# Kernel optimization log

Hardware: AMD Instinct MI355X
Metric: run time of the kernel (lower is better)

## Reference

```python
import jax, jax.numpy as jnp
import numpy as np

V, D, L, H, F, S = 32000, 1024, 6, 16, 4096, 1024
B, T = 2, 1024
DH = D // H
EPS = 1e-5


def layer_norm(x, w, b):
    m = jnp.mean(x, axis=-1, keepdims=True)
    v = jnp.var(x, axis=-1, keepdims=True)
    return (x - m) * jax.lax.rsqrt(v + EPS) * w + b


def setup_inputs() -> dict:
    key = jax.random.key(0)
    ks = jax.random.split(key, 12)
    n = lambda k, shape: jax.random.normal(k, shape, jnp.float32) * 0.02
    return {
        "idx": jax.random.randint(ks[0], (B, T), 0, V),
        "tok_emb": n(ks[1], (V, D)),
        "pos_emb": n(ks[2], (S, D)),
        "ln1_w": jnp.ones((L, D), jnp.float32),
        "ln1_b": jnp.zeros((L, D), jnp.float32),
        "wq": n(ks[3], (L, D, D)),
        "wk": n(ks[4], (L, D, D)),
        "wv": n(ks[5], (L, D, D)),
        "proj": n(ks[6], (L, D, D)),
        "ln2_w": jnp.ones((L, D), jnp.float32),
        "ln2_b": jnp.zeros((L, D), jnp.float32),
        "fc1_w": n(ks[7], (L, F, D)),
        "fc1_b": jnp.zeros((L, F), jnp.float32),
        "fc2_w": n(ks[8], (L, D, F)),
        "fc2_b": jnp.zeros((L, D), jnp.float32),
        "lnf_w": jnp.ones((D,), jnp.float32),
        "lnf_b": jnp.zeros((D,), jnp.float32),
        "head_w": n(ks[9], (V, D)),
    }


def reference(idx, tok_emb, pos_emb, ln1_w, ln1_b, wq, wk, wv, proj,
              ln2_w, ln2_b, fc1_w, fc1_b, fc2_w, fc2_b, lnf_w, lnf_b, head_w):
    b, t = idx.shape
    x = tok_emb[idx] + pos_emb[:t][None, :, :]  # [B,T,D]
    causal = jnp.tril(jnp.ones((t, t), bool))

    def block(x, p):
        l1w, l1b, Wq, Wk, Wv, Wp, l2w, l2b, F1w, F1b, F2w, F2b = p
        h = layer_norm(x, l1w, l1b)
        q = (h @ Wq.T).reshape(b, t, H, DH).transpose(0, 2, 1, 3)  # [B,H,T,dh]
        k = (h @ Wk.T).reshape(b, t, H, DH).transpose(0, 2, 1, 3)
        v = (h @ Wv.T).reshape(b, t, H, DH).transpose(0, 2, 1, 3)
        # muP attention: 1/d_head scaling (not 1/sqrt(d_head))
        att = jnp.einsum('bhqd,bhkd->bhqk', q, k) * (1.0 / DH)
        att = jnp.where(causal, att, -jnp.inf)
        att = jax.nn.softmax(att, axis=-1)
        y = jnp.einsum('bhqk,bhkd->bhqd', att, v)
        y = y.transpose(0, 2, 1, 3).reshape(b, t, D)
        x = x + y @ Wp.T
        h = layer_norm(x, l2w, l2b)
        h = jax.nn.gelu(h @ F1w.T + F1b, approximate=False)  # torch F.gelu = exact erf
        x = x + (h @ F2w.T + F2b)
        return x, None

    x, _ = jax.lax.scan(block, x, (ln1_w, ln1_b, wq, wk, wv, proj,
                                   ln2_w, ln2_b, fc1_w, fc1_b, fc2_w, fc2_b))
    x = layer_norm(x, lnf_w, lnf_b)
    return x @ head_w.T  # [B,T,V] logits (MuReadout with unit multipliers)
```

## Files before the change

kernel.cpp:

```cpp
#include <hip/hip_runtime.h>
#include <cmath>

typedef __bf16 bf16_t;
typedef bf16_t bf16x8 __attribute__((ext_vector_type(8)));
typedef bf16_t bf16x4 __attribute__((ext_vector_type(4)));
typedef float floatx4 __attribute__((ext_vector_type(4)));

#define B_ 2
#define T_ 1024
#define D_ 1024
#define H_ 16
#define DH_ 64
#define L_ 6
#define F_ 4096
#define V_ 32000
#define NTOK (B_ * T_)

__global__ __launch_bounds__(256) void detect_kernel(
    const unsigned short* __restrict__ tok, int* __restrict__ flag)
{
  __shared__ int cnt;
  if (threadIdx.x == 0) cnt = 0;
  __syncthreads();
  int c = 0;
#pragma unroll
  for (int i = 0; i < 16; i++) {
    unsigned short h = tok[threadIdx.x * 16 + i];
    int e = (h >> 7) & 0xFF;
    if (e >= 134) c++;
  }
  atomicAdd(&cnt, c);
  __syncthreads();
  if (threadIdx.x == 0) *flag = (cnt > 64) ? 1 : 0;
}

__device__ inline bf16x8 load8(const void* p, size_t i, int fp32m) {
  bf16x8 r;
  if (fp32m) {
    const float* f = (const float*)p + i;
    float4 v0 = *(const float4*)f;
    float4 v1 = *(const float4*)(f + 4);
    r[0] = (bf16_t)v0.x; r[1] = (bf16_t)v0.y; r[2] = (bf16_t)v0.z; r[3] = (bf16_t)v0.w;
    r[4] = (bf16_t)v1.x; r[5] = (bf16_t)v1.y; r[6] = (bf16_t)v1.z; r[7] = (bf16_t)v1.w;
  } else {
    r = *(const bf16x8*)((const bf16_t*)p + i);
  }
  return r;
}

__device__ inline float loadf(const void* p, size_t i, int fp32m) {
  return fp32m ? ((const float*)p)[i] : (float)((const bf16_t*)p)[i];
}

__global__ __launch_bounds__(256) void convflat_kernel(
    const void* __restrict__ src, bf16_t* __restrict__ dst,
    const int* __restrict__ modep, long n)
{
  int fp32m = *modep;
  size_t i = ((size_t)blockIdx.x * 256 + threadIdx.x) * 8;
  if ((long)i >= n) return;
  bf16x8 r = load8(src, i, fp32m);
  *(bf16x8*)(dst + i) = r;
}

__global__ __launch_bounds__(256) void convqkv_kernel(
    const void* __restrict__ wq, const void* __restrict__ wk,
    const void* __restrict__ wv, bf16_t* __restrict__ dst,
    const int* __restrict__ modep)
{
  int fp32m = *modep;
  size_t i = ((size_t)blockIdx.x * 256 + threadIdx.x) * 8;
  const size_t per = (size_t)D_ * D_;
  int lm = (int)(i / per);
  size_t off = i - (size_t)lm * per;
  int l = lm / 3, mat = lm - l * 3;
  const void* src = (mat == 0) ? wq : ((mat == 1) ? wk : wv);
  bf16x8 r = load8(src, (size_t)l * per + off, fp32m);
  *(bf16x8*)(dst + i) = r;
}

__global__ __launch_bounds__(256) void embed_kernel(
    const int* __restrict__ idx, const void* __restrict__ tok,
    const void* __restrict__ pos, float* __restrict__ x,
    const int* __restrict__ modep)
{
  int fp32m = *modep;
  int row = blockIdx.x;
  int t = row & (T_ - 1);
  int tokid = idx[row];
  int c = threadIdx.x * 4;
  float tv[4], pv[4];
  if (fp32m) {
    float4 a = *(const float4*)((const float*)tok + (size_t)tokid * D_ + c);
    float4 b = *(const float4*)((const float*)pos + (size_t)t * D_ + c);
    tv[0] = a.x; tv[1] = a.y; tv[2] = a.z; tv[3] = a.w;
    pv[0] = b.x; pv[1] = b.y; pv[2] = b.z; pv[3] = b.w;
  } else {
    bf16x4 a = *(const bf16x4*)((const bf16_t*)tok + (size_t)tokid * D_ + c);
    bf16x4 b = *(const bf16x4*)((const bf16_t*)pos + (size_t)t * D_ + c);
#pragma unroll
    for (int j = 0; j < 4; j++) { tv[j] = (float)a[j]; pv[j] = (float)b[j]; }
  }
  float4 o;
  o.x = tv[0] + pv[0]; o.y = tv[1] + pv[1];
  o.z = tv[2] + pv[2]; o.w = tv[3] + pv[3];
  *(float4*)(x + (size_t)row * D_ + c) = o;
}

__global__ __launch_bounds__(256) void ln_kernel(
    const float* __restrict__ x, const void* __restrict__ w,
    const void* __restrict__ bb, bf16_t* __restrict__ out,
    const int* __restrict__ modep, int woff)
{
  int fp32m = *modep;
  int row = blockIdx.x, tid = threadIdx.x;
  int lane = tid & 63, wid = tid >> 6;
  const float* xr = x + (size_t)row * D_;
  float4 xv = ((const float4*)xr)[tid];
  float s = xv.x + xv.y + xv.z + xv.w;
  float sq = xv.x * xv.x + xv.y * xv.y + xv.z * xv.z + xv.w * xv.w;
#pragma unroll
  for (int off = 32; off; off >>= 1) {
    s += __shfl_xor(s, off);
    sq += __shfl_xor(sq, off);
  }
  __shared__ float ss[4], ssq[4];
  if (lane == 0) { ss[wid] = s; ssq[wid] = sq; }
  __syncthreads();
  s = ss[0] + ss[1] + ss[2] + ss[3];
  sq = ssq[0] + ssq[1] + ssq[2] + ssq[3];
  float mean = s * (1.f / D_);
  float var = sq * (1.f / D_) - mean * mean;
  var = fmaxf(var, 0.f);
  float rstd = rsqrtf(var + 1e-5f);
  int c = tid * 4;
  float xa[4] = {xv.x, xv.y, xv.z, xv.w};
  bf16x4 ov;
#pragma unroll
  for (int j = 0; j < 4; j++) {
    float wj = loadf(w, (size_t)woff + c + j, fp32m);
    float bj = loadf(bb, (size_t)woff + c + j, fp32m);
    ov[j] = (bf16_t)((xa[j] - mean) * rstd * wj + bj);
  }
  *(bf16x4*)(out + (size_t)row * D_ + c) = ov;
}

__device__ inline float gelu_f(float v) {
  return 0.5f * v * (1.f + erff(v * 0.70710678118654752f));
}

__device__ inline void gload16(void* lds, const void* g) {
  __builtin_amdgcn_global_load_lds(
      (__attribute__((address_space(1))) void*)(g),
      (__attribute__((address_space(3))) void*)(lds), 16, 0, 0);
}

__global__ __launch_bounds__(256) void gemm128(
    const bf16_t* __restrict__ A, const bf16_t* __restrict__ W,
    const void* __restrict__ bias, size_t boff, const float* __restrict__ res,
    bf16_t* __restrict__ outb, float* __restrict__ outf, void* __restrict__ outx,
    const int* __restrict__ modep, int M, int N, int K, int dogelu)
{
  __shared__ __align__(16) bf16_t As[128 * 32];
  __shared__ __align__(16) bf16_t Bs[128 * 32];
  int fp32m = *modep;
  int tid = threadIdx.x;
  int lane = tid & 63, wid = tid >> 6;
  int wm = wid & 1, wn = wid >> 1;
  int m0 = blockIdx.x * 128, n0 = blockIdx.y * 128;
  int ln15 = lane & 15, q4 = lane >> 4;
  int srow = tid >> 2;
  int scol = (tid & 3) * 8;
  const bf16_t* Ag0 = A + (size_t)(m0 + srow) * K + scol;
  const bf16_t* Ag1 = A + (size_t)(m0 + 64 + srow) * K + scol;
  const bf16_t* Wg0 = W + (size_t)(n0 + srow) * K + scol;
  const bf16_t* Wg1 = W + (size_t)(n0 + 64 + srow) * K + scol;
  bf16_t* Asp0 = &As[tid * 8];
  bf16_t* Asp1 = &As[2048 + tid * 8];
  bf16_t* Bsp0 = &Bs[tid * 8];
  bf16_t* Bsp1 = &Bs[2048 + tid * 8];
  floatx4 acc[4][4] = {};
  for (int k0 = 0; k0 < K; k0 += 32) {
    __syncthreads();
    gload16(Asp0, Ag0 + k0);
    gload16(Asp1, Ag1 + k0);
    gload16(Bsp0, Wg0 + k0);
    gload16(Bsp1, Wg1 + k0);
    __syncthreads();
    bf16x8 a[4], b[4];
#pragma unroll
    for (int i = 0; i < 4; i++) {
      a[i] = *(const bf16x8*)&As[(wm * 64 + i * 16 + ln15) * 32 + q4 * 8];
      b[i] = *(const bf16x8*)&Bs[(wn * 64 + i * 16 + ln15) * 32 + q4 * 8];
    }
#pragma unroll
    for (int mt = 0; mt < 4; mt++)
#pragma unroll
      for (int nt = 0; nt < 4; nt++)
        acc[mt][nt] = __builtin_amdgcn_mfma_f32_16x16x32_bf16(a[mt], b[nt], acc[mt][nt], 0, 0, 0);
  }
#pragma unroll
  for (int mt = 0; mt < 4; mt++)
#pragma unroll
    for (int nt = 0; nt < 4; nt++) {
      int col = n0 + wn * 64 + nt * 16 + ln15;
      float bv = bias ? loadf(bias, boff + col, fp32m) : 0.f;
#pragma unroll
      for (int r = 0; r < 4; r++) {
        int row = m0 + wm * 64 + mt * 16 + q4 * 4 + r;
        float v = acc[mt][nt][r] + bv;
        if (dogelu) v = gelu_f(v);
        size_t o = (size_t)row * N + col;
        if (res) v += res[o];
        if (outf) outf[o] = v;
        if (outb) outb[o] = (bf16_t)v;
        if (outx) {
          if (fp32m) ((float*)outx)[o] = v;
          else ((bf16_t*)outx)[o] = (bf16_t)v;
        }
      }
    }
}

__global__ __launch_bounds__(256) void gemm_bt(
    const bf16_t* __restrict__ A, const void* __restrict__ W, size_t woffs,
    const void* __restrict__ bias, size_t boff, const float* __restrict__ res,
    bf16_t* __restrict__ outb, float* __restrict__ outf, void* __restrict__ outx,
    const int* __restrict__ modep, int M, int N, int K, int dogelu)
{
  __shared__ __align__(16) bf16_t As[64][40];
  __shared__ __align__(16) bf16_t Bs[64][40];
  int fp32m = *modep;
  int tid = threadIdx.x;
  int lane = tid & 63, wid = tid >> 6;
  int wm = wid & 1, wn = wid >> 1;
  int m0 = blockIdx.y * 64, n0 = blockIdx.x * 64;
  int srow = tid >> 2, scol = (tid & 3) * 8;
  const bf16_t* Ap = A + (size_t)(m0 + srow) * K + scol;
  size_t wrow = woffs + (size_t)(n0 + srow) * K + scol;
  floatx4 acc[2][2] = {};
  int ln15 = lane & 15, q4 = lane >> 4;
  for (int k0 = 0; k0 < K; k0 += 32) {
    __syncthreads();
    *(bf16x8*)&As[srow][scol] = *(const bf16x8*)(Ap + k0);
    *(bf16x8*)&Bs[srow][scol] = load8(W, wrow + k0, fp32m);
    __syncthreads();
    bf16x8 a0 = *(const bf16x8*)&As[wm * 32 + ln15][q4 * 8];
    bf16x8 a1 = *(const bf16x8*)&As[wm * 32 + 16 + ln15][q4 * 8];
    bf16x8 b0 = *(const bf16x8*)&Bs[wn * 32 + ln15][q4 * 8];
    bf16x8 b1 = *(const bf16x8*)&Bs[wn * 32 + 16 + ln15][q4 * 8];
    acc[0][0] = __builtin_amdgcn_mfma_f32_16x16x32_bf16(a0, b0, acc[0][0], 0, 0, 0);
    acc[0][1] = __builtin_amdgcn_mfma_f32_16x16x32_bf16(a0, b1, acc[0][1], 0, 0, 0);
    acc[1][0] = __builtin_amdgcn_mfma_f32_16x16x32_bf16(a1, b0, acc[1][0], 0, 0, 0);
    acc[1][1] = __builtin_amdgcn_mfma_f32_16x16x32_bf16(a1, b1, acc[1][1], 0, 0, 0);
  }
#pragma unroll
  for (int mt = 0; mt < 2; mt++)
#pragma unroll
    for (int nt = 0; nt < 2; nt++) {
      int col = n0 + wn * 32 + nt * 16 + ln15;
      float bv = bias ? loadf(bias, boff + col, fp32m) : 0.f;
#pragma unroll
      for (int r = 0; r < 4; r++) {
        int row = m0 + wm * 32 + mt * 16 + q4 * 4 + r;
        float v = acc[mt][nt][r] + bv;
        if (dogelu) v = gelu_f(v);
        size_t o = (size_t)row * N + col;
        if (res) v += res[o];
        if (outf) outf[o] = v;
        if (outb) outb[o] = (bf16_t)v;
        if (outx) {
          if (fp32m) ((float*)outx)[o] = v;
          else ((bf16_t*)outx)[o] = (bf16_t)v;
        }
      }
    }
}

__global__ __launch_bounds__(256) void attn_mfma(
    const bf16_t* __restrict__ qkv, bf16_t* __restrict__ y)
{
  __shared__ __align__(16) bf16_t Ks[64][72];
  __shared__ __align__(16) bf16_t Vt[64][72];
  __shared__ __align__(16) bf16_t Ps[4][16][72];
  int tid = threadIdx.x;
  int lane = tid & 63, w = tid >> 6;
  int ln15 = lane & 15, g = lane >> 4;
  int idxb = blockIdx.x;
  int phase = idxb >> 8, slot = idxb & 255;
  int bh = slot >> 3, jj = slot & 7;
  int qb = phase ? jj : (15 - jj);
  int b = bh >> 4, h = bh & 15;
  int q0 = qb * 64;
  int qrow = q0 + w * 16;
  const bf16_t* kp = qkv + 1024;
  const bf16_t* vp = qkv + 2048;
  bf16x8 qa0, qa1;
  {
    size_t base = ((size_t)(b * T_ + qrow + ln15)) * 3072 + h * 64 + g * 8;
    qa0 = *(const bf16x8*)(qkv + base);
    qa1 = *(const bf16x8*)(qkv + base + 32);
  }
  floatx4 o[4] = {};
  float m_i[4], l_i[4];
#pragma unroll
  for (int r = 0; r < 4; r++) { m_i[r] = -__builtin_inff(); l_i[r] = 0.f; }
  int ntile = qb + 1;
  int sr = tid >> 2, sc = (tid & 3) * 16;
  for (int it = 0; it < ntile; it++) {
    int k0 = it * 64;
    __syncthreads();
    size_t gb = ((size_t)(b * T_ + k0 + sr)) * 3072 + h * 64 + sc;
    bf16x8 kv0 = *(const bf16x8*)(kp + gb);
    bf16x8 kv1 = *(const bf16x8*)(kp + gb + 8);
    bf16x8 vv0 = *(const bf16x8*)(vp + gb);
    bf16x8 vv1 = *(const bf16x8*)(vp + gb + 8);
    *(bf16x8*)&Ks[sr][sc] = kv0;
    *(bf16x8*)&Ks[sr][sc + 8] = kv1;
#pragma unroll
    for (int e = 0; e < 8; e++) {
      int d0 = sc + e, d1 = sc + 8 + e;
      Vt[d0][sr ^ (((d0 >> 3) & 7) << 3)] = vv0[e];
      Vt[d1][sr ^ (((d1 >> 3) & 7) << 3)] = vv1[e];
    }
    __syncthreads();
    floatx4 s[4] = {};
#pragma unroll
    for (int nt = 0; nt < 4; nt++) {
      bf16x8 b0 = *(const bf16x8*)&Ks[nt * 16 + ln15][g * 8];
      bf16x8 b1 = *(const bf16x8*)&Ks[nt * 16 + ln15][32 + g * 8];
      s[nt] = __builtin_amdgcn_mfma_f32_16x16x32_bf16(qa0, b0, s[nt], 0, 0, 0);
      s[nt] = __builtin_amdgcn_mfma_f32_16x16x32_bf16(qa1, b1, s[nt], 0, 0, 0);
    }
    int last = (it == ntile - 1);
    float p[4][4];
    float mt[4];
#pragma unroll
    for (int r = 0; r < 4; r++) mt[r] = -__builtin_inff();
#pragma unroll
    for (int nt = 0; nt < 4; nt++)
#pragma unroll
      for (int r = 0; r < 4; r++) {
        float sv = s[nt][r] * 0.015625f;
        if (last && (k0 + nt * 16 + ln15) > (qrow + g * 4 + r))
          sv = -__builtin_inff();
        p[nt][r] = sv;
        mt[r] = fmaxf(mt[r], sv);
      }
#pragma unroll
    for (int off = 1; off < 16; off <<= 1)
#pragma unroll
      for (int r = 0; r < 4; r++) mt[r] = fmaxf(mt[r], __shfl_xor(mt[r], off));
    float alpha[4];
#pragma unroll
    for (int r = 0; r < 4; r++) {
      float mn = fmaxf(m_i[r], mt[r]);
      alpha[r] = __expf(m_i[r] - mn);
      m_i[r] = mn;
    }
    float rs[4] = {0.f, 0.f, 0.f, 0.f};
#pragma unroll
    for (int nt = 0; nt < 4; nt++)
#pragma unroll
      for (int r = 0; r < 4; r++) {
        float pv = __expf(p[nt][r] - m_i[r]);
        rs[r] += pv;
        Ps[w][g * 4 + r][nt * 16 + ln15] = (bf16_t)pv;
      }
#pragma unroll
    for (int off = 1; off < 16; off <<= 1)
#pragma unroll
      for (int r = 0; r < 4; r++) rs[r] += __shfl_xor(rs[r], off);
#pragma unroll
    for (int r = 0; r < 4; r++) l_i[r] = l_i[r] * alpha[r] + rs[r];
#pragma unroll
    for (int nt = 0; nt < 4; nt++)
#pragma unroll
      for (int r = 0; r < 4; r++) o[nt][r] *= alpha[r];
#pragma unroll
    for (int ks = 0; ks < 2; ks++) {
      bf16x8 pa = *(const bf16x8*)&Ps[w][ln15][ks * 32 + g * 8];
#pragma unroll
      for (int nt = 0; nt < 4; nt++) {
        int d = nt * 16 + ln15;
        bf16x8 vb = *(const bf16x8*)&Vt[d][(ks * 32 + g * 8) ^ (((d >> 3) & 7) << 3)];
        o[nt] = __builtin_amdgcn_mfma_f32_16x16x32_bf16(pa, vb, o[nt], 0, 0, 0);
      }
    }
  }
#pragma unroll
  for (int nt = 0; nt < 4; nt++)
#pragma unroll
    for (int r = 0; r < 4; r++) {
      size_t orow = (size_t)(b * T_ + qrow + g * 4 + r) * D_ + h * 64 + nt * 16 + ln15;
      y[orow] = (bf16_t)(o[nt][r] / l_i[r]);
    }
}

__global__ __launch_bounds__(256) void attn_kernel(
    const bf16_t* __restrict__ q, const bf16_t* __restrict__ k,
    const bf16_t* __restrict__ v, bf16_t* __restrict__ y, int stride)
{
  __shared__ float Kt[64][65];
  __shared__ float Vt[64][65];
  __shared__ float qs[4][64];
  __shared__ float ps[4][64];
  int tid = threadIdx.x;
  int lane = tid & 63, w = tid >> 6;
  int blk = blockIdx.x;
  int tqblk = blk & 255;
  int bh = blk >> 8;
  int b = bh >> 4, hh = bh & 15;
  int tq_base = tqblk * 4;
  int tq = tq_base + w;
  size_t qrow = ((size_t)(b * T_ + tq)) * stride + hh * DH_;
  qs[w][lane] = (float)q[qrow + lane];
  float m_i = -INFINITY, l_i = 0.f, acc = 0.f;
  int ntiles = (tq_base >> 6) + 1;
  int lr = tid >> 2, lc = (tid & 3) * 16;
  for (int it = 0; it < ntiles; it++) {
    int tk0 = it * 64;
    __syncthreads();
    size_t gbase = ((size_t)(b * T_ + tk0 + lr)) * stride + hh * DH_ + lc;
    bf16x8 kv0 = *(const bf16x8*)(k + gbase);
    bf16x8 kv1 = *(const bf16x8*)(k + gbase + 8);
    bf16x8 vv0 = *(const bf16x8*)(v + gbase);
    bf16x8 vv1 = *(const bf16x8*)(v + gbase + 8);
#pragma unroll
    for (int j = 0; j < 8; j++) {
      Kt[lr][lc + j] = (float)kv0[j];
      Kt[lr][lc + 8 + j] = (float)kv1[j];
      Vt[lr][lc + j] = (float)vv0[j];
      Vt[lr][lc + 8 + j] = (float)vv1[j];
    }
    __syncthreads();
    int tk = tk0 + lane;
    float s = -INFINITY;
    if (tk <= tq) {
      float a = 0.f;
#pragma unroll
      for (int d = 0; d < 64; d++) a += qs[w][d] * Kt[lane][d];
      s = a * (1.f / 64.f);
    }
    float mt = s;
#pragma unroll
    for (int off = 32; off; off >>= 1) mt = fmaxf(mt, __shfl_xor(mt, off));
    float mnew = fmaxf(m_i, mt);
    float alpha = (m_i == -INFINITY) ? 0.f : expf(m_i - mnew);
    float p = (tk <= tq) ? expf(s - mnew) : 0.f;
    float psum = p;
#pragma unroll
    for (int off = 32; off; off >>= 1) psum += __shfl_xor(psum, off);
    l_i = l_i * alpha + psum;
    ps[w][lane] = p;
    float pv = 0.f;
#pragma unroll
    for (int j = 0; j < 64; j++) pv += ps[w][j] * Vt[j][lane];
    acc = acc * alpha + pv;
    m_i = mnew;
  }
  y[((size_t)(b * T_ + tq)) * D_ + hh * DH_ + lane] = (bf16_t)(acc / l_i);
}

static inline void launch_gemm128(const bf16_t* A, const bf16_t* W,
                                  const void* bias, size_t boff, const float* res,
                                  bf16_t* outb, float* outf, void* outx,
                                  const int* modep, int M, int N, int K,
                                  int dogelu, hipStream_t s)
{
  dim3 g(M / 128, N / 128);
  gemm128<<<g, dim3(256), 0, s>>>(A, W, bias, boff, res, outb, outf, outx,
                                  modep, M, N, K, dogelu);
}

static inline void launch_gemm_old(const bf16_t* A, const void* W, size_t woffs,
                                   const void* bias, size_t boff, const float* res,
                                   bf16_t* outb, float* outf, void* outx,
                                   const int* modep, int M, int N, int K,
                                   int dogelu, hipStream_t s)
{
  dim3 g(N / 64, M / 64);
  gemm_bt<<<g, dim3(256), 0, s>>>(A, W, woffs, bias, boff, res, outb, outf,
                                  outx, modep, M, N, K, dogelu);
}

#define OFF_X      256ull
#define OFF_H      8388864ull
#define OFF_QKV    12583168ull
#define OFF_Y      25166080ull
#define OFF_HF     29360384ull
#define OFF_WQKV   46137600ull
#define OFF_WPROJ  83886336ull
#define OFF_WFC1   96469248ull
#define OFF_WFC2   146800896ull
#define OFF_WHEAD  197132544ull
#define REQ_WS     262668544ull

extern "C" void kernel_launch(void* const* d_in, const int* in_sizes, int n_in,
                              void* d_out, int out_size, void* d_ws, size_t ws_size,
                              hipStream_t stream)
{
  (void)in_sizes; (void)n_in; (void)out_size;
  const int* idx      = (const int*)d_in[0];
  const void* tok_emb = d_in[1];
  const void* pos_emb = d_in[2];
  const void* ln1_w   = d_in[3];
  const void* ln1_b   = d_in[4];
  const void* wq      = d_in[5];
  const void* wk      = d_in[6];
  const void* wv      = d_in[7];
  const void* wproj   = d_in[8];
  const void* ln2_w   = d_in[9];
  const void* ln2_b   = d_in[10];
  const void* fc1_w   = d_in[11];
  const void* fc1_b   = d_in[12];
  const void* fc2_w   = d_in[13];
  const void* fc2_b   = d_in[14];
  const void* lnf_w   = d_in[15];
  const void* lnf_b   = d_in[16];
  const void* head_w  = d_in[17];

  char* ws = (char*)d_ws;
  int* modep = (int*)ws;
  detect_kernel<<<1, 256, 0, stream>>>((const unsigned short*)tok_emb, modep);

  if (ws_size >= REQ_WS) {
    float*  x   = (float*)(ws + OFF_X);
    bf16_t* h   = (bf16_t*)(ws + OFF_H);
    bf16_t* qkv = (bf16_t*)(ws + OFF_QKV);
    bf16_t* yb  = (bf16_t*)(ws + OFF_Y);
    bf16_t* hf  = (bf16_t*)(ws + OFF_HF);
    bf16_t* wqkvb = (bf16_t*)(ws + OFF_WQKV);
    bf16_t* wprjb = (bf16_t*)(ws + OFF_WPROJ);
    bf16_t* wfc1b = (bf16_t*)(ws + OFF_WFC1);
    bf16_t* wfc2b = (bf16_t*)(ws + OFF_WFC2);
    bf16_t* whedb = (bf16_t*)(ws + OFF_WHEAD);

    convqkv_kernel<<<9216, 256, 0, stream>>>(wq, wk, wv, wqkvb, modep);
    convflat_kernel<<<3072, 256, 0, stream>>>(wproj, wprjb, modep, (long)L_ * D_ * D_);
    convflat_kernel<<<12288, 256, 0, stream>>>(fc1_w, wfc1b, modep, (long)L_ * F_ * D_);
    convflat_kernel<<<12288, 256, 0, stream>>>(fc2_w, wfc2b, modep, (long)L_ * D_ * F_);
    convflat_kernel<<<16000, 256, 0, stream>>>(head_w, whedb, modep, (long)V_ * D_);

    embed_kernel<<<NTOK, 256, 0, stream>>>(idx, tok_emb, pos_emb, x, modep);

    for (int l = 0; l < L_; l++) {
      size_t wd = (size_t)l * D_ * D_;
      size_t wf = (size_t)l * F_ * D_;
      ln_kernel<<<NTOK, 256, 0, stream>>>(x, ln1_w, ln1_b, h, modep, l * D_);
      launch_gemm128(h, wqkvb + (size_t)l * 3 * D_ * D_, nullptr, 0, nullptr,
                     qkv, nullptr, nullptr, modep, NTOK, 3 * D_, D_, 0, stream);
      attn_mfma<<<512, 256, 0, stream>>>(qkv, yb);
      launch_gemm128(yb, wprjb + wd, nullptr, 0, x, nullptr, x, nullptr,
                     modep, NTOK, D_, D_, 0, stream);
      ln_kernel<<<NTOK, 256, 0, stream>>>(x, ln2_w, ln2_b, h, modep, l * D_);
      launch_gemm128(h, wfc1b + wf, fc1_b, (size_t)l * F_, nullptr, hf, nullptr,
                     nullptr, modep, NTOK, F_, D_, 1, stream);
      launch_gemm128(hf, wfc2b + wf, fc2_b, (size_t)l * D_, x, nullptr, x,
                     nullptr, modep, NTOK, D_, F_, 0, stream);
    }

    ln_kernel<<<NTOK, 256, 0, stream>>>(x, lnf_w, lnf_b, h, modep, 0);
    launch_gemm128(h, whedb, nullptr, 0, nullptr, nullptr, nullptr, d_out,
                   modep, NTOK, V_, D_, 0, stream);
  } else {
    float*  x  = (float*)(ws + 256);
    bf16_t* h  = (bf16_t*)(ws + 8388864);
    bf16_t* qb = (bf16_t*)(ws + 12583168);
    bf16_t* kb = (bf16_t*)(ws + 16777472);
    bf16_t* vb = (bf16_t*)(ws + 20971776);
    bf16_t* yb = (bf16_t*)(ws + 25166080);
    bf16_t* hf = (bf16_t*)(ws + 29360384);

    embed_kernel<<<NTOK, 256, 0, stream>>>(idx, tok_emb, pos_emb, x, modep);

    for (int l = 0; l < L_; l++) {
      size_t wd = (size_t)l * D_ * D_;
      size_t wf = (size_t)l * F_ * D_;
      ln_kernel<<<NTOK, 256, 0, stream>>>(x, ln1_w, ln1_b, h, modep, l * D_);
      launch_gemm_old(h, wq, wd, nullptr, 0, nullptr, qb, nullptr, nullptr,
                      modep, NTOK, D_, D_, 0, stream);
      launch_gemm_old(h, wk, wd, nullptr, 0, nullptr, kb, nullptr, nullptr,
                      modep, NTOK, D_, D_, 0, stream);
      launch_gemm_old(h, wv, wd, nullptr, 0, nullptr, vb, nullptr, nullptr,
                      modep, NTOK, D_, D_, 0, stream);
      attn_kernel<<<B_ * H_ * (T_ / 4), 256, 0, stream>>>(qb, kb, vb, yb, D_);
      launch_gemm_old(yb, wproj, wd, nullptr, 0, x, nullptr, x, nullptr,
                      modep, NTOK, D_, D_, 0, stream);
      ln_kernel<<<NTOK, 256, 0, stream>>>(x, ln2_w, ln2_b, h, modep, l * D_);
      launch_gemm_old(h, fc1_w, wf, fc1_b, (size_t)l * F_, nullptr, hf, nullptr,
                      nullptr, modep, NTOK, F_, D_, 1, stream);
      launch_gemm_old(hf, fc2_w, wf, fc2_b, (size_t)l * D_, x, nullptr, x,
                      nullptr, modep, NTOK, D_, F_, 0, stream);
    }

    ln_kernel<<<NTOK, 256, 0, stream>>>(x, lnf_w, lnf_b, h, modep, 0);
    launch_gemm_old(h, head_w, 0, nullptr, 0, nullptr, nullptr, nullptr, d_out,
                    modep, NTOK, V_, D_, 0, stream);
  }
}
```

Measured before the change: 2.644 ms.

## Template GEMM tile sizes and remap workgroups across XCDs for L2 locality

Turns the fixed 128x128 GEMM into a BM x BN template and gives each projection its own tile shape: smaller tiles for the narrow-N projection and fc2 GEMMs, so they launch more workgroups on the many CUs. It also switches to a 1D grid whose block ids are remapped so consecutive workgroups on the same XCD cover neighbouring M tiles of one N column, aiming for better L2 reuse of weight tiles. Smaller tiles cost more reloads of operands per FLOP and lower MFMA density per wave.

```diff
diff --git a/kernel.cpp b/kernel.cpp
--- a/kernel.cpp
+++ b/kernel.cpp
@@ -155,59 +155,68 @@
       (__attribute__((address_space(3))) void*)(lds), 16, 0, 0);
 }
 
-__global__ __launch_bounds__(256) void gemm128(
+template<int BM, int BN>
+__global__ __launch_bounds__(256) void gemm_t(
     const bf16_t* __restrict__ A, const bf16_t* __restrict__ W,
     const void* __restrict__ bias, size_t boff, const float* __restrict__ res,
     bf16_t* __restrict__ outb, float* __restrict__ outf, void* __restrict__ outx,
-    const int* __restrict__ modep, int M, int N, int K, int dogelu)
-{
-  __shared__ __align__(16) bf16_t As[128 * 32];
-  __shared__ __align__(16) bf16_t Bs[128 * 32];
+    const int* __restrict__ modep, int M, int N, int K, int dogelu, int mshift)
+{
+  constexpr int MT = BM / 32, NT = BN / 32;
+  __shared__ __align__(16) bf16_t As[BM * 32];
+  __shared__ __align__(16) bf16_t Bs[BN * 32];
   int fp32m = *modep;
   int tid = threadIdx.x;
   int lane = tid & 63, wid = tid >> 6;
   int wm = wid & 1, wn = wid >> 1;
-  int m0 = blockIdx.x * 128, n0 = blockIdx.y * 128;
+  int nwg = gridDim.x, bid = blockIdx.x;
+  int qq = nwg >> 3, rr = nwg & 7;
+  int xcd = bid & 7, ii = bid >> 3;
+  int wg = (xcd < rr ? xcd * (qq + 1) : rr * (qq + 1) + (xcd - rr) * qq) + ii;
+  int m0 = (wg & ((1 << mshift) - 1)) * BM;
+  int n0 = (wg >> mshift) * BN;
   int ln15 = lane & 15, q4 = lane >> 4;
-  int srow = tid >> 2;
-  int scol = (tid & 3) * 8;
-  const bf16_t* Ag0 = A + (size_t)(m0 + srow) * K + scol;
-  const bf16_t* Ag1 = A + (size_t)(m0 + 64 + srow) * K + scol;
-  const bf16_t* Wg0 = W + (size_t)(n0 + srow) * K + scol;
-  const bf16_t* Wg1 = W + (size_t)(n0 + 64 + srow) * K + scol;
-  bf16_t* Asp0 = &As[tid * 8];
-  bf16_t* Asp1 = &As[2048 + tid * 8];
-  bf16_t* Bsp0 = &Bs[tid * 8];
-  bf16_t* Bsp1 = &Bs[2048 + tid * 8];
-  floatx4 acc[4][4] = {};
+  int srow = tid >> 2, scol = (tid & 3) * 8;
+  const bf16_t* Ag[BM / 64];
+  const bf16_t* Wg[BN / 64];
+#pragma unroll
+  for (int hh = 0; hh < BM / 64; hh++)
+    Ag[hh] = A + (size_t)(m0 + hh * 64 + srow) * K + scol;
+#pragma unroll
+  for (int hh = 0; hh < BN / 64; hh++)
+    Wg[hh] = W + (size_t)(n0 + hh * 64 + srow) * K + scol;
+  floatx4 acc[MT][NT] = {};
   for (int k0 = 0; k0 < K; k0 += 32) {
     __syncthreads();
-    gload16(Asp0, Ag0 + k0);
-    gload16(Asp1, Ag1 + k0);
-    gload16(Bsp0, Wg0 + k0);
-    gload16(Bsp1, Wg1 + k0);
-    __syncthreads();
-    bf16x8 a[4], b[4];
-#pragma unroll
-    for (int i = 0; i < 4; i++) {
-      a[i] = *(const bf16x8*)&As[(wm * 64 + i * 16 + ln15) * 32 + q4 * 8];
-      b[i] = *(const bf16x8*)&Bs[(wn * 64 + i * 16 + ln15) * 32 + q4 * 8];
-    }
-#pragma unroll
-    for (int mt = 0; mt < 4; mt++)
-#pragma unroll
-      for (int nt = 0; nt < 4; nt++)
+#pragma unroll
+    for (int hh = 0; hh < BM / 64; hh++)
+      gload16(&As[hh * 2048 + tid * 8], Ag[hh] + k0);
+#pragma unroll
+    for (int hh = 0; hh < BN / 64; hh++)
+      gload16(&Bs[hh * 2048 + tid * 8], Wg[hh] + k0);
+    __syncthreads();
+    bf16x8 a[MT], b[NT];
+#pragma unroll
+    for (int i = 0; i < MT; i++)
+      a[i] = *(const bf16x8*)&As[(wm * (BM / 2) + i * 16 + ln15) * 32 + q4 * 8];
+#pragma unroll
+    for (int j = 0; j < NT; j++)
+      b[j] = *(const bf16x8*)&Bs[(wn * (BN / 2) + j * 16 + ln15) * 32 + q4 * 8];
+#pragma unroll
+    for (int mt = 0; mt < MT; mt++)
+#pragma unroll
+      for (int nt = 0; nt < NT; nt++)
         acc[mt][nt] = __builtin_amdgcn_mfma_f32_16x16x32_bf16(a[mt], b[nt], acc[mt][nt], 0, 0, 0);
   }
 #pragma unroll
-  for (int mt = 0; mt < 4; mt++)
-#pragma unroll
-    for (int nt = 0; nt < 4; nt++) {
-      int col = n0 + wn * 64 + nt * 16 + ln15;
+  for (int mt = 0; mt < MT; mt++)
+#pragma unroll
+    for (int nt = 0; nt < NT; nt++) {
+      int col = n0 + wn * (BN / 2) + nt * 16 + ln15;
       float bv = bias ? loadf(bias, boff + col, fp32m) : 0.f;
 #pragma unroll
       for (int r = 0; r < 4; r++) {
-        int row = m0 + wm * 64 + mt * 16 + q4 * 4 + r;
+        int row = m0 + wm * (BM / 2) + mt * 16 + q4 * 4 + r;
         float v = acc[mt][nt][r] + bv;
         if (dogelu) v = gelu_f(v);
         size_t o = (size_t)row * N + col;
@@ -462,15 +471,18 @@
   y[((size_t)(b * T_ + tq)) * D_ + hh * DH_ + lane] = (bf16_t)(acc / l_i);
 }
 
-static inline void launch_gemm128(const bf16_t* A, const bf16_t* W,
-                                  const void* bias, size_t boff, const float* res,
-                                  bf16_t* outb, float* outf, void* outx,
-                                  const int* modep, int M, int N, int K,
-                                  int dogelu, hipStream_t s)
-{
-  dim3 g(M / 128, N / 128);
-  gemm128<<<g, dim3(256), 0, s>>>(A, W, bias, boff, res, outb, outf, outx,
-                                  modep, M, N, K, dogelu);
+template<int BM, int BN>
+static inline void launch_gemm_t(const bf16_t* A, const bf16_t* W,
+                                 const void* bias, size_t boff, const float* res,
+                                 bf16_t* outb, float* outf, void* outx,
+                                 const int* modep, int M, int N, int K,
+                                 int dogelu, hipStream_t s)
+{
+  int nMB = M / BM;
+  int mshift = (nMB == 16) ? 4 : ((nMB == 32) ? 5 : 31 - __builtin_clz(nMB));
+  int nwg = nMB * (N / BN);
+  gemm_t<BM, BN><<<dim3(nwg), dim3(256), 0, s>>>(
+      A, W, bias, boff, res, outb, outf, outx, modep, M, N, K, dogelu, mshift);
 }
 
 static inline void launch_gemm_old(const bf16_t* A, const void* W, size_t woffs,
@@ -548,21 +560,22 @@
       size_t wd = (size_t)l * D_ * D_;
       size_t wf = (size_t)l * F_ * D_;
       ln_kernel<<<NTOK, 256, 0, stream>>>(x, ln1_w, ln1_b, h, modep, l * D_);
-      launch_gemm128(h, wqkvb + (size_t)l * 3 * D_ * D_, nullptr, 0, nullptr,
-                     qkv, nullptr, nullptr, modep, NTOK, 3 * D_, D_, 0, stream);
+      launch_gemm_t<64, 128>(h, wqkvb + (size_t)l * 3 * D_ * D_, nullptr, 0,
+                             nullptr, qkv, nullptr, nullptr, modep,
+                             NTOK, 3 * D_, D_, 0, stream);
       attn_mfma<<<512, 256, 0, stream>>>(qkv, yb);
-      launch_gemm128(yb, wprjb + wd, nullptr, 0, x, nullptr, x, nullptr,
-                     modep, NTOK, D_, D_, 0, stream);
+      launch_gemm_t<64, 64>(yb, wprjb + wd, nullptr, 0, x, nullptr, x, nullptr,
+                            modep, NTOK, D_, D_, 0, stream);
       ln_kernel<<<NTOK, 256, 0, stream>>>(x, ln2_w, ln2_b, h, modep, l * D_);
-      launch_gemm128(h, wfc1b + wf, fc1_b, (size_t)l * F_, nullptr, hf, nullptr,
-                     nullptr, modep, NTOK, F_, D_, 1, stream);
-      launch_gemm128(hf, wfc2b + wf, fc2_b, (size_t)l * D_, x, nullptr, x,
-                     nullptr, modep, NTOK, D_, F_, 0, stream);
+      launch_gemm_t<128, 128>(h, wfc1b + wf, fc1_b, (size_t)l * F_, nullptr, hf,
+                              nullptr, nullptr, modep, NTOK, F_, D_, 1, stream);
+      launch_gemm_t<64, 64>(hf, wfc2b + wf, fc2_b, (size_t)l * D_, x, nullptr, x,
+                            nullptr, modep, NTOK, D_, F_, 0, stream);
     }
 
     ln_kernel<<<NTOK, 256, 0, stream>>>(x, lnf_w, lnf_b, h, modep, 0);
-    launch_gemm128(h, whedb, nullptr, 0, nullptr, nullptr, nullptr, d_out,
-                   modep, NTOK, V_, D_, 0, stream);
+    launch_gemm_t<128, 128>(h, whedb, nullptr, 0, nullptr, nullptr, nullptr,
+                            d_out, modep, NTOK, V_, D_, 0, stream);
   } else {
     float*  x  = (float*)(ws + 256);
     bf16_t* h  = (bf16_t*)(ws + 8388864);
```

New measurement: 2.319 ms. 12.3% less time.
